# Performance work log

Hardware: AMD Instinct MI355X
Metric: run time of the kernel (lower is better)

The kernel has to match this reference:

```python
import jax, jax.numpy as jnp
import numpy as np

N_NODES = 100000


def _gcn_conv(x, src, dst, ew, W, b, n_nodes):
    # PyG GCNConv: x' = D^{-1/2} (A + I) D^{-1/2} (x W) + b, with edge weights.
    h = x @ W  # [N, out]
    deg = jax.ops.segment_sum(ew, dst, num_segments=n_nodes)  # weighted in-degree
    dinv = jnp.where(deg > 0, jax.lax.rsqrt(deg), 0.0)
    norm = dinv[src] * ew * dinv[dst]  # [E]
    msg = h[src] * norm[:, None]  # gather + scale
    out = jax.ops.segment_sum(msg, dst, num_segments=n_nodes)  # scatter-add
    return out + b


def setup_inputs() -> dict:
    key = jax.random.key(0)
    ks = jax.random.split(key, 10)
    E = 1600000
    D_IN, H1, H2, D_OUT = 512, 128, 64, 1
    x = jax.random.normal(ks[0], (N_NODES, D_IN), dtype=jnp.float32)
    edge_index = jax.random.randint(ks[1], (2, E), 0, N_NODES, dtype=jnp.int64)
    edge_attr = jax.random.uniform(ks[2], (E,), dtype=jnp.float32)
    def glorot(k, fan_in, fan_out):
        s = jnp.sqrt(6.0 / (fan_in + fan_out))
        return jax.random.uniform(k, (fan_in, fan_out), minval=-s, maxval=s, dtype=jnp.float32)
    return {
        "x": x,
        "edge_index": edge_index,
        "edge_attr": edge_attr,
        "W1": glorot(ks[3], D_IN, H1), "b1": jnp.zeros((H1,), jnp.float32),
        "W2": glorot(ks[4], H1, H2), "b2": jnp.zeros((H2,), jnp.float32),
        "W3": glorot(ks[5], H2, D_OUT), "b3": jnp.zeros((D_OUT,), jnp.float32),
    }


def reference(x, edge_index, edge_attr, W1, b1, W2, b2, W3, b3):
    n = x.shape[0]
    # add self-loops with weight 1 (PyG GCNConv default)
    loops = jnp.arange(n, dtype=edge_index.dtype)
    src = jnp.concatenate([edge_index[0], loops])
    dst = jnp.concatenate([edge_index[1], loops])
    ew = jnp.concatenate([edge_attr, jnp.ones((n,), edge_attr.dtype)])
    h = _gcn_conv(x, src, dst, ew, W1, b1, n)
    h = jax.nn.relu(h)  # dropout is identity in eval mode
    h = _gcn_conv(h, src, dst, ew, W2, b2, n)
    h = jax.nn.relu(h)
    out = _gcn_conv(h, src, dst, ew, W3, b3, n)
    return out
```

## Files before the change

kernel.cpp:

```cpp
#include <hip/hip_runtime.h>

typedef __attribute__((ext_vector_type(4))) float f32x4;
typedef __attribute__((ext_vector_type(8))) short bf16x8;
typedef __attribute__((ext_vector_type(4))) unsigned short u16x4;

__device__ __forceinline__ unsigned short f2bf(float f) {
  unsigned int u = __builtin_bit_cast(unsigned int, f);
  u += 0x7fffu + ((u >> 16) & 1u);
  return (unsigned short)(u >> 16);
}
__device__ __forceinline__ float bf2f(unsigned short h) {
  unsigned int u = ((unsigned int)h) << 16;
  return __builtin_bit_cast(float, u);
}
__device__ __forceinline__ float bflo(unsigned int u) { return bf2f((unsigned short)(u & 0xffffu)); }
__device__ __forceinline__ float bfhi(unsigned int u) { return bf2f((unsigned short)(u >> 16)); }

__global__ void hist_rank_k(const int* __restrict__ dst, int* __restrict__ cnt,
                            int* __restrict__ rank, int E) {
  int e = blockIdx.x * blockDim.x + threadIdx.x;
  if (e < E) rank[e] = atomicAdd(&cnt[dst[e]], 1);
}

__global__ void scan1_k(const int* __restrict__ cnt, int* __restrict__ row,
                        int* __restrict__ bsum, int N) {
  __shared__ int sh[256];
  const int tid = threadIdx.x;
  const int base = blockIdx.x * 2048 + tid * 8;
  int v[8]; int s = 0;
#pragma unroll
  for (int i = 0; i < 8; ++i) {
    int idx = base + i;
    v[i] = (idx < N) ? cnt[idx] : 0;
    s += v[i];
  }
  sh[tid] = s;
  __syncthreads();
  for (int off = 1; off < 256; off <<= 1) {
    int t = (tid >= off) ? sh[tid - off] : 0;
    __syncthreads();
    sh[tid] += t;
    __syncthreads();
  }
  int excl = sh[tid] - s;
  if (tid == 255) bsum[blockIdx.x] = sh[255];
  int run = excl;
#pragma unroll
  for (int i = 0; i < 8; ++i) {
    int idx = base + i;
    if (idx < N) row[idx] = run;
    run += v[i];
  }
}
__global__ void scan2_k(int* __restrict__ bsum, int nb) {
  if (threadIdx.x == 0 && blockIdx.x == 0) {
    int run = 0;
    for (int i = 0; i < nb; ++i) { int t = bsum[i]; bsum[i] = run; run += t; }
  }
}
__global__ void scan3_k(int* __restrict__ row, const int* __restrict__ bsum, int N, int E) {
  int idx = blockIdx.x * blockDim.x + threadIdx.x;
  if (idx < N) row[idx] += bsum[idx >> 11];
  if (idx == N) row[N] = E;
}
__global__ void scatter_nr_k(const int* __restrict__ src, const int* __restrict__ dst,
                             const float* __restrict__ ew, const int* __restrict__ row,
                             const int* __restrict__ rank, uint2* __restrict__ eadj, int E) {
  int e = blockIdx.x * blockDim.x + threadIdx.x;
  if (e >= E) return;
  int pos = row[dst[e]] + rank[e];
  eadj[pos] = make_uint2((unsigned)src[e], __builtin_bit_cast(unsigned, ew[e]));
}
__global__ void deg_dinv_k(const int* __restrict__ row, const uint2* __restrict__ eadj,
                           float* __restrict__ dinv, int N) {
  int n = blockIdx.x * blockDim.x + threadIdx.x;
  if (n >= N) return;
  float s = 1.0f;
  int end = row[n + 1];
  for (int e = row[n]; e < end; ++e) s += __builtin_bit_cast(float, eadj[e].y);
  dinv[n] = rsqrtf(s);
}
__global__ void fixnorm_k(const int* __restrict__ row, uint2* __restrict__ eadj,
                          const float* __restrict__ dinv, int N) {
  int n = blockIdx.x * blockDim.x + threadIdx.x;
  if (n >= N) return;
  float dd = dinv[n];
  int end = row[n + 1];
  for (int e = row[n]; e < end; ++e) {
    uint2 m = eadj[e];
    float nm = __builtin_bit_cast(float, m.y) * dinv[m.x] * dd;
    eadj[e].y = __builtin_bit_cast(unsigned, nm);
  }
}
__global__ void conv_wt2_k(const float* __restrict__ W1, unsigned short* __restrict__ Wt1,
                           const float* __restrict__ W2, unsigned short* __restrict__ Wt2) {
  int idx = blockIdx.x * blockDim.x + threadIdx.x;
  if (idx < 512 * 128) {
    int n = idx >> 9, k = idx & 511;
    Wt1[idx] = f2bf(W1[k * 128 + n]);
  } else {
    int j = idx - 512 * 128;
    if (j < 128 * 64) {
      int n = j >> 7, k = j & 127;
      Wt2[j] = f2bf(W2[k * 64 + n]);
    }
  }
}

template<int NC, int KD, bool RELU>
__launch_bounds__(256, 2)
__global__ void gemm_k(const float* __restrict__ A, const unsigned short* __restrict__ Wt,
                       unsigned short* __restrict__ Hb, int M) {
  constexpr int BM = 128, BK = 64;
  constexpr int WN = 64;
  constexpr int WGN = NC / WN;
  constexpr int WGM = 4 / WGN;
  constexpr int WM = BM / WGM;
  constexpr int FM = WM / 16;
  constexpr int FN = WN / 16;
  constexpr int KSUB = BK / 32;
  constexpr int A_PER_T = BM * (BK / 4) / 256;
  constexpr int B_PER_T = NC * (BK / 8) / 256;
  constexpr int nT = KD / BK;

  __shared__ unsigned short As[BM * BK];
  __shared__ unsigned short Bs[NC * BK];
  char* asb = reinterpret_cast<char*>(As);
  char* bsb = reinterpret_cast<char*>(Bs);

  const int tid = threadIdx.x;
  const int lane = tid & 63;
  const int wid = tid >> 6;
  const int wr = wid / WGN;
  const int wc = wid % WGN;
  const int lg = lane >> 4;
  const int lr = lane & 15;
  const int blockM = blockIdx.x * BM;

  float4 areg[A_PER_T];
  uint4 breg[B_PER_T];

  auto load_tiles = [&](int k0) {
#pragma unroll
    for (int i = 0; i < A_PER_T; ++i) {
      int chunk = tid + i * 256;
      int r = chunk >> 4, c4 = chunk & 15;
      int gr = blockM + r; if (gr >= M) gr = M - 1;
      areg[i] = *reinterpret_cast<const float4*>(A + (size_t)gr * KD + k0 + c4 * 4);
    }
#pragma unroll
    for (int i = 0; i < B_PER_T; ++i) {
      int chunk = tid + i * 256;
      int n = chunk >> 3, c = chunk & 7;
      breg[i] = *reinterpret_cast<const uint4*>(Wt + (size_t)n * KD + k0 + c * 8);
    }
  };

  f32x4 acc[FM][FN] = {};
  load_tiles(0);

  for (int t = 0; t < nT; ++t) {
    __syncthreads();
#pragma unroll
    for (int i = 0; i < A_PER_T; ++i) {
      int chunk = tid + i * 256;
      int r = chunk >> 4, c4 = chunk & 15;
      float4 v = areg[i];
      if (RELU) {
        v.x = fmaxf(v.x, 0.f); v.y = fmaxf(v.y, 0.f);
        v.z = fmaxf(v.z, 0.f); v.w = fmaxf(v.w, 0.f);
      }
      u16x4 p = { f2bf(v.x), f2bf(v.y), f2bf(v.z), f2bf(v.w) };
      int byte = r * (BK * 2) + ((c4 * 8) ^ ((r & 7) << 4));
      *reinterpret_cast<u16x4*>(asb + byte) = p;
    }
#pragma unroll
    for (int i = 0; i < B_PER_T; ++i) {
      int chunk = tid + i * 256;
      int n = chunk >> 3, c = chunk & 7;
      int byte = n * (BK * 2) + ((c * 16) ^ ((n & 7) << 4));
      *reinterpret_cast<uint4*>(bsb + byte) = breg[i];
    }
    __syncthreads();
    if (t + 1 < nT) load_tiles((t + 1) * BK);

    bf16x8 af[FM][KSUB], bfr[FN][KSUB];
#pragma unroll
    for (int fm = 0; fm < FM; ++fm)
#pragma unroll
      for (int kk = 0; kk < KSUB; ++kk) {
        int row = wr * WM + fm * 16 + lr;
        int k = kk * 32 + lg * 8;
        int byte = row * (BK * 2) + ((k * 2) ^ ((row & 7) << 4));
        af[fm][kk] = *reinterpret_cast<const bf16x8*>(asb + byte);
      }
#pragma unroll
    for (int fn = 0; fn < FN; ++fn)
#pragma unroll
      for (int kk = 0; kk < KSUB; ++kk) {
        int n = wc * WN + fn * 16 + lr;
        int k = kk * 32 + lg * 8;
        int byte = n * (BK * 2) + ((k * 2) ^ ((n & 7) << 4));
        bfr[fn][kk] = *reinterpret_cast<const bf16x8*>(bsb + byte);
      }
#pragma unroll
    for (int kk = 0; kk < KSUB; ++kk)
#pragma unroll
      for (int fm = 0; fm < FM; ++fm)
#pragma unroll
        for (int fn = 0; fn < FN; ++fn)
          acc[fm][fn] = __builtin_amdgcn_mfma_f32_16x16x32_bf16(
              af[fm][kk], bfr[fn][kk], acc[fm][fn], 0, 0, 0);
  }

#pragma unroll
  for (int fm = 0; fm < FM; ++fm) {
#pragma unroll
    for (int fn = 0; fn < FN; ++fn) {
      int col = wc * WN + fn * 16 + lr;
#pragma unroll
      for (int j = 0; j < 4; ++j) {
        int row = blockM + wr * WM + fm * 16 + lg * 4 + j;
        if (row < M)
          Hb[(size_t)row * NC + col] = f2bf(acc[fm][fn][j]);
      }
    }
  }
}

__global__ void agg_csr128_k(const int* __restrict__ row, const uint2* __restrict__ eadj,
                             const unsigned short* __restrict__ h, const float* __restrict__ bias,
                             const float* __restrict__ dinv, float* __restrict__ out, int N) {
  const int lane = threadIdx.x & 63;
  const int node = blockIdx.x * (blockDim.x >> 6) + (threadIdx.x >> 6);
  if (node >= N) return;
  const int beg = row[node], end = row[node + 1];
  const float di = dinv[node];
  unsigned int hv = *reinterpret_cast<const unsigned int*>(h + (size_t)node * 128 + lane * 2);
  float acc0 = bflo(hv) * di * di;
  float acc1 = bfhi(hv) * di * di;
  int e = beg;
  for (; e + 2 <= end; e += 2) {
    uint2 m0 = eadj[e], m1 = eadj[e + 1];
    int s0 = __builtin_amdgcn_readfirstlane(m0.x);
    int s1 = __builtin_amdgcn_readfirstlane(m1.x);
    float n0 = __builtin_bit_cast(float, __builtin_amdgcn_readfirstlane(m0.y));
    float n1 = __builtin_bit_cast(float, __builtin_amdgcn_readfirstlane(m1.y));
    unsigned int h0 = *reinterpret_cast<const unsigned int*>(h + (size_t)s0 * 128 + lane * 2);
    unsigned int h1 = *reinterpret_cast<const unsigned int*>(h + (size_t)s1 * 128 + lane * 2);
    acc0 += bflo(h0) * n0 + bflo(h1) * n1;
    acc1 += bfhi(h0) * n0 + bfhi(h1) * n1;
  }
  if (e < end) {
    uint2 m0 = eadj[e];
    int s0 = __builtin_amdgcn_readfirstlane(m0.x);
    float n0 = __builtin_bit_cast(float, __builtin_amdgcn_readfirstlane(m0.y));
    unsigned int h0 = *reinterpret_cast<const unsigned int*>(h + (size_t)s0 * 128 + lane * 2);
    acc0 += bflo(h0) * n0;
    acc1 += bfhi(h0) * n0;
  }
  float2 b = *reinterpret_cast<const float2*>(bias + lane * 2);
  float2 o = { acc0 + b.x, acc1 + b.y };
  *reinterpret_cast<float2*>(out + (size_t)node * 128 + lane * 2) = o;
}

__global__ void agg_csr64_k(const int* __restrict__ row, const uint2* __restrict__ eadj,
                            const unsigned short* __restrict__ h, const float* __restrict__ bias,
                            const float* __restrict__ dinv, float* __restrict__ out, int N) {
  const int lane = threadIdx.x & 63;
  const int half = lane >> 5;
  const int l = lane & 31;
  const int node = blockIdx.x * (blockDim.x >> 6) + (threadIdx.x >> 6);
  if (node >= N) return;
  const int beg = row[node], end = row[node + 1];
  float acc0 = 0.f, acc1 = 0.f;
  if (half == 0) {
    const float di = dinv[node];
    unsigned int hv = *reinterpret_cast<const unsigned int*>(h + (size_t)node * 64 + l * 2);
    acc0 = bflo(hv) * di * di;
    acc1 = bfhi(hv) * di * di;
  }
  for (int e = beg + half; e < end; e += 2) {
    uint2 m = eadj[e];
    int s = m.x;
    float nm = __builtin_bit_cast(float, m.y);
    unsigned int hv = *reinterpret_cast<const unsigned int*>(h + (size_t)s * 64 + l * 2);
    acc0 += bflo(hv) * nm;
    acc1 += bfhi(hv) * nm;
  }
  acc0 += __shfl_xor(acc0, 32, 64);
  acc1 += __shfl_xor(acc1, 32, 64);
  if (half == 0) {
    float2 b = *reinterpret_cast<const float2*>(bias + l * 2);
    float2 o = { acc0 + b.x, acc1 + b.y };
    *reinterpret_cast<float2*>(out + (size_t)node * 64 + l * 2) = o;
  }
}

__global__ void agg_csr1_k(const int* __restrict__ row, const uint2* __restrict__ eadj,
                           const float* __restrict__ h3, const float* __restrict__ b3,
                           const float* __restrict__ dinv, float* __restrict__ out, int N) {
  int n = blockIdx.x * blockDim.x + threadIdx.x;
  if (n >= N) return;
  float di = dinv[n];
  float acc = h3[n] * di * di;
  int end = row[n + 1];
  for (int e = row[n]; e < end; ++e) {
    uint2 m = eadj[e];
    acc += h3[m.x] * __builtin_bit_cast(float, m.y);
  }
  out[n] = acc + b3[0];
}

__global__ void gemv3_k(const float* __restrict__ o2, const float* __restrict__ W3,
                        float* __restrict__ h3, int M) {
  int lane = threadIdx.x & 63;
  int r = blockIdx.x * (blockDim.x >> 6) + (threadIdx.x >> 6);
  if (r >= M) return;
  float v = fmaxf(o2[(size_t)r * 64 + lane], 0.f) * W3[lane];
#pragma unroll
  for (int off = 32; off > 0; off >>= 1) v += __shfl_xor(v, off, 64);
  if (lane == 0) h3[r] = v;
}

extern "C" void kernel_launch(void* const* d_in, const int* in_sizes, int n_in,
                              void* d_out, int out_size, void* d_ws, size_t ws_size,
                              hipStream_t stream) {
  const float* x  = (const float*)d_in[0];
  const int*   ei = (const int*)d_in[1];
  const float* ea = (const float*)d_in[2];
  const float* W1 = (const float*)d_in[3];
  const float* b1 = (const float*)d_in[4];
  const float* W2 = (const float*)d_in[5];
  const float* b2 = (const float*)d_in[6];
  const float* W3 = (const float*)d_in[7];
  const float* b3 = (const float*)d_in[8];
  float* out = (float*)d_out;

  const int N = in_sizes[0] / 512;
  const int E = in_sizes[2];
  const int* src = ei;
  const int* dst = ei + E;

  char* w = (char*)d_ws;
  auto alloc = [&](size_t bytes) {
    char* p = w; w += (bytes + 511) & ~(size_t)511; return p;
  };
  float* dinv         = (float*)alloc((size_t)N * 4);
  int*   cnt          = (int*)alloc((size_t)N * 4);
  int*   rowp         = (int*)alloc((size_t)(N + 1) * 4);
  int*   bsum         = (int*)alloc(4096 * 4);
  int*   rank         = (int*)alloc((size_t)E * 4);
  uint2* eadj         = (uint2*)alloc((size_t)E * 8);
  unsigned short* h1  = (unsigned short*)alloc((size_t)N * 128 * 2);
  float* o1           = (float*)alloc((size_t)N * 128 * 4);
  unsigned short* h2  = (unsigned short*)alloc((size_t)N * 64 * 2);
  float* o2           = (float*)alloc((size_t)N * 64 * 4);
  float* h3           = (float*)alloc((size_t)N * 4);
  unsigned short* wt1 = (unsigned short*)alloc(512 * 128 * 2);
  unsigned short* wt2 = (unsigned short*)alloc(128 * 64 * 2);

  const int TB = 256;
  const int nb_scan = (N + 2047) / 2048;

  hipMemsetAsync(cnt, 0, (size_t)N * 4, stream);

  hist_rank_k<<<(E + TB - 1) / TB, TB, 0, stream>>>(dst, cnt, rank, E);
  scan1_k<<<nb_scan, 256, 0, stream>>>(cnt, rowp, bsum, N);
  scan2_k<<<1, 64, 0, stream>>>(bsum, nb_scan);
  scan3_k<<<(N + 1 + TB - 1) / TB, TB, 0, stream>>>(rowp, bsum, N, E);
  scatter_nr_k<<<(E + TB - 1) / TB, TB, 0, stream>>>(src, dst, ea, rowp, rank, eadj, E);
  deg_dinv_k<<<(N + TB - 1) / TB, TB, 0, stream>>>(rowp, eadj, dinv, N);
  fixnorm_k<<<(N + TB - 1) / TB, TB, 0, stream>>>(rowp, eadj, dinv, N);
  conv_wt2_k<<<(512 * 128 + 128 * 64 + TB - 1) / TB, TB, 0, stream>>>(W1, wt1, W2, wt2);

  const int gblocks = (N + 127) / 128;
  const int ablocks = (N + 3) / 4;
  gemm_k<128, 512, false><<<gblocks, TB, 0, stream>>>(x, wt1, h1, N);
  agg_csr128_k<<<ablocks, TB, 0, stream>>>(rowp, eadj, h1, b1, dinv, o1, N);
  gemm_k<64, 128, true><<<gblocks, TB, 0, stream>>>(o1, wt2, h2, N);
  agg_csr64_k<<<ablocks, TB, 0, stream>>>(rowp, eadj, h2, b2, dinv, o2, N);
  gemv3_k<<<ablocks, TB, 0, stream>>>(o2, W3, h3, N);
  agg_csr1_k<<<(N + TB - 1) / TB, TB, 0, stream>>>(rowp, eadj, h3, b3, dinv, out, N);
}
```

Baseline: 713.1 us.

## Fuse ReLU/bf16 into layer-1 aggregation and layer-2 aggregation with W3 GEMV

```diff
diff --git a/kernel.cpp b/kernel.cpp
--- a/kernel.cpp
+++ b/kernel.cpp
@@ -15,6 +15,9 @@
 }
 __device__ __forceinline__ float bflo(unsigned int u) { return bf2f((unsigned short)(u & 0xffffu)); }
 __device__ __forceinline__ float bfhi(unsigned int u) { return bf2f((unsigned short)(u >> 16)); }
+__device__ __forceinline__ unsigned int packbf(float a, float b) {
+  return (unsigned int)f2bf(a) | ((unsigned int)f2bf(b) << 16);
+}
 
 __global__ void hist_rank_k(const int* __restrict__ dst, int* __restrict__ cnt,
                             int* __restrict__ rank, int E) {
@@ -107,10 +110,10 @@
   }
 }
 
-template<int NC, int KD, bool RELU>
+template<int NC, int KD>
 __launch_bounds__(256, 2)
-__global__ void gemm_k(const float* __restrict__ A, const unsigned short* __restrict__ Wt,
-                       unsigned short* __restrict__ Hb, int M) {
+__global__ void gemm_f32a_k(const float* __restrict__ A, const unsigned short* __restrict__ Wt,
+                            unsigned short* __restrict__ Hb, int M) {
   constexpr int BM = 128, BK = 64;
   constexpr int WN = 64;
   constexpr int WGN = NC / WN;
@@ -166,10 +169,6 @@
       int chunk = tid + i * 256;
       int r = chunk >> 4, c4 = chunk & 15;
       float4 v = areg[i];
-      if (RELU) {
-        v.x = fmaxf(v.x, 0.f); v.y = fmaxf(v.y, 0.f);
-        v.z = fmaxf(v.z, 0.f); v.w = fmaxf(v.w, 0.f);
-      }
       u16x4 p = { f2bf(v.x), f2bf(v.y), f2bf(v.z), f2bf(v.w) };
       int byte = r * (BK * 2) + ((c4 * 8) ^ ((r & 7) << 4));
       *reinterpret_cast<u16x4*>(asb + byte) = p;
@@ -214,7 +213,7 @@
   }
 
 #pragma unroll
-  for (int fm = 0; fm < FM; ++fm) {
+  for (int fm = 0; fm < FM; ++fm)
 #pragma unroll
     for (int fn = 0; fn < FN; ++fn) {
       int col = wc * WN + fn * 16 + lr;
@@ -225,76 +224,204 @@
           Hb[(size_t)row * NC + col] = f2bf(acc[fm][fn][j]);
       }
     }
-  }
+}
+
+__launch_bounds__(256, 2)
+__global__ void gemm_bf16a_k(const unsigned short* __restrict__ A,
+                             const unsigned short* __restrict__ Wt,
+                             unsigned short* __restrict__ Hb, int M) {
+  constexpr int BM = 128, BK = 64, NC = 64, KD = 128;
+  constexpr int WM = 32;
+  constexpr int FM = 2, FN = 4, KSUB = 2;
+  constexpr int A_PER_T = 4;
+  constexpr int B_PER_T = 2;
+  constexpr int nT = KD / BK;
+
+  __shared__ unsigned short As[BM * BK];
+  __shared__ unsigned short Bs[NC * BK];
+  char* asb = reinterpret_cast<char*>(As);
+  char* bsb = reinterpret_cast<char*>(Bs);
+
+  const int tid = threadIdx.x;
+  const int lane = tid & 63;
+  const int wid = tid >> 6;
+  const int lg = lane >> 4;
+  const int lr = lane & 15;
+  const int blockM = blockIdx.x * BM;
+
+  uint4 areg[A_PER_T];
+  uint4 breg[B_PER_T];
+
+  auto load_tiles = [&](int k0) {
+#pragma unroll
+    for (int i = 0; i < A_PER_T; ++i) {
+      int chunk = tid + i * 256;
+      int r = chunk >> 3, c = chunk & 7;
+      int gr = blockM + r; if (gr >= M) gr = M - 1;
+      areg[i] = *reinterpret_cast<const uint4*>(A + (size_t)gr * KD + k0 + c * 8);
+    }
+#pragma unroll
+    for (int i = 0; i < B_PER_T; ++i) {
+      int chunk = tid + i * 256;
+      int n = chunk >> 3, c = chunk & 7;
+      breg[i] = *reinterpret_cast<const uint4*>(Wt + (size_t)n * KD + k0 + c * 8);
+    }
+  };
+
+  f32x4 acc[FM][FN] = {};
+  load_tiles(0);
+
+  for (int t = 0; t < nT; ++t) {
+    __syncthreads();
+#pragma unroll
+    for (int i = 0; i < A_PER_T; ++i) {
+      int chunk = tid + i * 256;
+      int r = chunk >> 3, c = chunk & 7;
+      int byte = r * (BK * 2) + ((c * 16) ^ ((r & 7) << 4));
+      *reinterpret_cast<uint4*>(asb + byte) = areg[i];
+    }
+#pragma unroll
+    for (int i = 0; i < B_PER_T; ++i) {
+      int chunk = tid + i * 256;
+      int n = chunk >> 3, c = chunk & 7;
+      int byte = n * (BK * 2) + ((c * 16) ^ ((n & 7) << 4));
+      *reinterpret_cast<uint4*>(bsb + byte) = breg[i];
+    }
+    __syncthreads();
+    if (t + 1 < nT) load_tiles((t + 1) * BK);
+
+    bf16x8 af[FM][KSUB], bfr[FN][KSUB];
+#pragma unroll
+    for (int fm = 0; fm < FM; ++fm)
+#pragma unroll
+      for (int kk = 0; kk < KSUB; ++kk) {
+        int row = wid * WM + fm * 16 + lr;
+        int k = kk * 32 + lg * 8;
+        int byte = row * (BK * 2) + ((k * 2) ^ ((row & 7) << 4));
+        af[fm][kk] = *reinterpret_cast<const bf16x8*>(asb + byte);
+      }
+#pragma unroll
+    for (int fn = 0; fn < FN; ++fn)
+#pragma unroll
+      for (int kk = 0; kk < KSUB; ++kk) {
+        int n = fn * 16 + lr;
+        int k = kk * 32 + lg * 8;
+        int byte = n * (BK * 2) + ((k * 2) ^ ((n & 7) << 4));
+        bfr[fn][kk] = *reinterpret_cast<const bf16x8*>(bsb + byte);
+      }
+#pragma unroll
+    for (int kk = 0; kk < KSUB; ++kk)
+#pragma unroll
+      for (int fm = 0; fm < FM; ++fm)
+#pragma unroll
+        for (int fn = 0; fn < FN; ++fn)
+          acc[fm][fn] = __builtin_amdgcn_mfma_f32_16x16x32_bf16(
+              af[fm][kk], bfr[fn][kk], acc[fm][fn], 0, 0, 0);
+  }
+
+#pragma unroll
+  for (int fm = 0; fm < FM; ++fm)
+#pragma unroll
+    for (int fn = 0; fn < FN; ++fn) {
+      int col = fn * 16 + lr;
+#pragma unroll
+      for (int j = 0; j < 4; ++j) {
+        int row = blockM + wid * WM + fm * 16 + lg * 4 + j;
+        if (row < M)
+          Hb[(size_t)row * NC + col] = f2bf(acc[fm][fn][j]);
+      }
+    }
 }
 
 __global__ void agg_csr128_k(const int* __restrict__ row, const uint2* __restrict__ eadj,
                              const unsigned short* __restrict__ h, const float* __restrict__ bias,
-                             const float* __restrict__ dinv, float* __restrict__ out, int N) {
+                             const float* __restrict__ dinv, unsigned int* __restrict__ o1b, int N) {
   const int lane = threadIdx.x & 63;
   const int node = blockIdx.x * (blockDim.x >> 6) + (threadIdx.x >> 6);
   if (node >= N) return;
+  const unsigned int* hu = reinterpret_cast<const unsigned int*>(h);
   const int beg = row[node], end = row[node + 1];
   const float di = dinv[node];
-  unsigned int hv = *reinterpret_cast<const unsigned int*>(h + (size_t)node * 128 + lane * 2);
-  float acc0 = bflo(hv) * di * di;
-  float acc1 = bfhi(hv) * di * di;
+  const float di2 = di * di;
+  unsigned int hv = hu[(size_t)node * 64 + lane];
+  float acc0 = bflo(hv) * di2;
+  float acc1 = bfhi(hv) * di2;
   int e = beg;
-  for (; e + 2 <= end; e += 2) {
-    uint2 m0 = eadj[e], m1 = eadj[e + 1];
+  for (; e + 4 <= end; e += 4) {
+    uint2 m0 = eadj[e], m1 = eadj[e + 1], m2 = eadj[e + 2], m3 = eadj[e + 3];
     int s0 = __builtin_amdgcn_readfirstlane(m0.x);
     int s1 = __builtin_amdgcn_readfirstlane(m1.x);
+    int s2 = __builtin_amdgcn_readfirstlane(m2.x);
+    int s3 = __builtin_amdgcn_readfirstlane(m3.x);
     float n0 = __builtin_bit_cast(float, __builtin_amdgcn_readfirstlane(m0.y));
     float n1 = __builtin_bit_cast(float, __builtin_amdgcn_readfirstlane(m1.y));
-    unsigned int h0 = *reinterpret_cast<const unsigned int*>(h + (size_t)s0 * 128 + lane * 2);
-    unsigned int h1 = *reinterpret_cast<const unsigned int*>(h + (size_t)s1 * 128 + lane * 2);
-    acc0 += bflo(h0) * n0 + bflo(h1) * n1;
-    acc1 += bfhi(h0) * n0 + bfhi(h1) * n1;
-  }
-  if (e < end) {
+    float n2 = __builtin_bit_cast(float, __builtin_amdgcn_readfirstlane(m2.y));
+    float n3 = __builtin_bit_cast(float, __builtin_amdgcn_readfirstlane(m3.y));
+    unsigned int h0 = hu[(size_t)s0 * 64 + lane];
+    unsigned int h1 = hu[(size_t)s1 * 64 + lane];
+    unsigned int h2 = hu[(size_t)s2 * 64 + lane];
+    unsigned int h3 = hu[(size_t)s3 * 64 + lane];
+    acc0 += bflo(h0) * n0 + bflo(h1) * n1 + bflo(h2) * n2 + bflo(h3) * n3;
+    acc1 += bfhi(h0) * n0 + bfhi(h1) * n1 + bfhi(h2) * n2 + bfhi(h3) * n3;
+  }
+  for (; e < end; ++e) {
     uint2 m0 = eadj[e];
     int s0 = __builtin_amdgcn_readfirstlane(m0.x);
     float n0 = __builtin_bit_cast(float, __builtin_amdgcn_readfirstlane(m0.y));
-    unsigned int h0 = *reinterpret_cast<const unsigned int*>(h + (size_t)s0 * 128 + lane * 2);
+    unsigned int h0 = hu[(size_t)s0 * 64 + lane];
     acc0 += bflo(h0) * n0;
     acc1 += bfhi(h0) * n0;
   }
-  float2 b = *reinterpret_cast<const float2*>(bias + lane * 2);
-  float2 o = { acc0 + b.x, acc1 + b.y };
-  *reinterpret_cast<float2*>(out + (size_t)node * 128 + lane * 2) = o;
-}
-
-__global__ void agg_csr64_k(const int* __restrict__ row, const uint2* __restrict__ eadj,
-                            const unsigned short* __restrict__ h, const float* __restrict__ bias,
-                            const float* __restrict__ dinv, float* __restrict__ out, int N) {
+  float2 b = reinterpret_cast<const float2*>(bias)[lane];
+  float r0 = fmaxf(acc0 + b.x, 0.f);
+  float r1 = fmaxf(acc1 + b.y, 0.f);
+  o1b[(size_t)node * 64 + lane] = packbf(r0, r1);
+}
+
+__global__ void agg_l23_k(const int* __restrict__ row, const uint2* __restrict__ eadj,
+                          const unsigned short* __restrict__ h2, const float* __restrict__ b2,
+                          const float* __restrict__ W3, const float* __restrict__ dinv,
+                          float* __restrict__ h3, int N) {
   const int lane = threadIdx.x & 63;
   const int half = lane >> 5;
   const int l = lane & 31;
   const int node = blockIdx.x * (blockDim.x >> 6) + (threadIdx.x >> 6);
   if (node >= N) return;
+  const unsigned int* hu = reinterpret_cast<const unsigned int*>(h2);
   const int beg = row[node], end = row[node + 1];
   float acc0 = 0.f, acc1 = 0.f;
-  if (half == 0) {
+  {
     const float di = dinv[node];
-    unsigned int hv = *reinterpret_cast<const unsigned int*>(h + (size_t)node * 64 + l * 2);
-    acc0 = bflo(hv) * di * di;
-    acc1 = bfhi(hv) * di * di;
-  }
-  for (int e = beg + half; e < end; e += 2) {
-    uint2 m = eadj[e];
-    int s = m.x;
-    float nm = __builtin_bit_cast(float, m.y);
-    unsigned int hv = *reinterpret_cast<const unsigned int*>(h + (size_t)s * 64 + l * 2);
-    acc0 += bflo(hv) * nm;
-    acc1 += bfhi(hv) * nm;
+    unsigned int hv = hu[(size_t)node * 32 + l];
+    float di2 = (half == 0) ? di * di : 0.f;
+    acc0 = bflo(hv) * di2;
+    acc1 = bfhi(hv) * di2;
+  }
+  int e = beg + half;
+  for (; e + 2 < end; e += 4) {
+    uint2 ma = eadj[e], mb = eadj[e + 2];
+    float na = __builtin_bit_cast(float, ma.y);
+    float nb = __builtin_bit_cast(float, mb.y);
+    unsigned int ha = hu[(size_t)ma.x * 32 + l];
+    unsigned int hb = hu[(size_t)mb.x * 32 + l];
+    acc0 += bflo(ha) * na + bflo(hb) * nb;
+    acc1 += bfhi(ha) * na + bfhi(hb) * nb;
+  }
+  if (e < end) {
+    uint2 ma = eadj[e];
+    float na = __builtin_bit_cast(float, ma.y);
+    unsigned int ha = hu[(size_t)ma.x * 32 + l];
+    acc0 += bflo(ha) * na;
+    acc1 += bfhi(ha) * na;
   }
   acc0 += __shfl_xor(acc0, 32, 64);
   acc1 += __shfl_xor(acc1, 32, 64);
-  if (half == 0) {
-    float2 b = *reinterpret_cast<const float2*>(bias + l * 2);
-    float2 o = { acc0 + b.x, acc1 + b.y };
-    *reinterpret_cast<float2*>(out + (size_t)node * 64 + l * 2) = o;
-  }
+  float2 bb = reinterpret_cast<const float2*>(b2)[l];
+  float2 w3 = reinterpret_cast<const float2*>(W3)[l];
+  float v = fmaxf(acc0 + bb.x, 0.f) * w3.x + fmaxf(acc1 + bb.y, 0.f) * w3.y;
+#pragma unroll
+  for (int off = 16; off > 0; off >>= 1) v += __shfl_xor(v, off, 64);
+  if (lane == 0) h3[node] = v;
 }
 
 __global__ void agg_csr1_k(const int* __restrict__ row, const uint2* __restrict__ eadj,
@@ -304,23 +431,18 @@
   if (n >= N) return;
   float di = dinv[n];
   float acc = h3[n] * di * di;
-  int end = row[n + 1];
-  for (int e = row[n]; e < end; ++e) {
+  const int beg = row[n], end = row[n + 1];
+  int e = beg;
+  for (; e + 2 <= end; e += 2) {
+    uint2 m0 = eadj[e], m1 = eadj[e + 1];
+    acc += h3[m0.x] * __builtin_bit_cast(float, m0.y)
+         + h3[m1.x] * __builtin_bit_cast(float, m1.y);
+  }
+  if (e < end) {
     uint2 m = eadj[e];
     acc += h3[m.x] * __builtin_bit_cast(float, m.y);
   }
   out[n] = acc + b3[0];
-}
-
-__global__ void gemv3_k(const float* __restrict__ o2, const float* __restrict__ W3,
-                        float* __restrict__ h3, int M) {
-  int lane = threadIdx.x & 63;
-  int r = blockIdx.x * (blockDim.x >> 6) + (threadIdx.x >> 6);
-  if (r >= M) return;
-  float v = fmaxf(o2[(size_t)r * 64 + lane], 0.f) * W3[lane];
-#pragma unroll
-  for (int off = 32; off > 0; off >>= 1) v += __shfl_xor(v, off, 64);
-  if (lane == 0) h3[r] = v;
 }
 
 extern "C" void kernel_launch(void* const* d_in, const int* in_sizes, int n_in,
@@ -353,9 +475,8 @@
   int*   rank         = (int*)alloc((size_t)E * 4);
   uint2* eadj         = (uint2*)alloc((size_t)E * 8);
   unsigned short* h1  = (unsigned short*)alloc((size_t)N * 128 * 2);
-  float* o1           = (float*)alloc((size_t)N * 128 * 4);
+  unsigned int* o1b   = (unsigned int*)alloc((size_t)N * 64 * 4);
   unsigned short* h2  = (unsigned short*)alloc((size_t)N * 64 * 2);
-  float* o2           = (float*)alloc((size_t)N * 64 * 4);
   float* h3           = (float*)alloc((size_t)N * 4);
   unsigned short* wt1 = (unsigned short*)alloc(512 * 128 * 2);
   unsigned short* wt2 = (unsigned short*)alloc(128 * 64 * 2);
@@ -376,10 +497,9 @@
 
   const int gblocks = (N + 127) / 128;
   const int ablocks = (N + 3) / 4;
-  gemm_k<128, 512, false><<<gblocks, TB, 0, stream>>>(x, wt1, h1, N);
-  agg_csr128_k<<<ablocks, TB, 0, stream>>>(rowp, eadj, h1, b1, dinv, o1, N);
-  gemm_k<64, 128, true><<<gblocks, TB, 0, stream>>>(o1, wt2, h2, N);
-  agg_csr64_k<<<ablocks, TB, 0, stream>>>(rowp, eadj, h2, b2, dinv, o2, N);
-  gemv3_k<<<ablocks, TB, 0, stream>>>(o2, W3, h3, N);
+  gemm_f32a_k<128, 512><<<gblocks, TB, 0, stream>>>(x, wt1, h1, N);
+  agg_csr128_k<<<ablocks, TB, 0, stream>>>(rowp, eadj, h1, b1, dinv, o1b, N);
+  gemm_bf16a_k<<<gblocks, TB, 0, stream>>>((const unsigned short*)o1b, wt2, h2, N);
+  agg_l23_k<<<ablocks, TB, 0, stream>>>(rowp, eadj, h2, b2, W3, dinv, h3, N);
   agg_csr1_k<<<(N + TB - 1) / TB, TB, 0, stream>>>(rowp, eadj, h3, b3, dinv, out, N);
 }
```

Measured after the change: 660.7 us. 1.08x faster.
